# Kernel tuning notes

Measured on AMD Instinct MI355X. Metric: run time of the kernel, lower is better.

Reference implementation:

```python
import jax, jax.numpy as jnp
import numpy as np

B = 1048576
INPUT_DIM = 64
NUM_LAYERS = 8   # number of trees
DEPTH = 6
TREE_DIM = 2
NUM_LEAVES = 2 ** DEPTH


def setup_inputs() -> dict:
    key = jax.random.key(0)
    ks = jax.random.split(key, 6)
    x = jax.random.normal(ks[0], (B, INPUT_DIM), dtype=jnp.float32)
    # Stacked per-tree, per-level Linear(input_dim, 1) selectors.
    W_sel = jax.random.normal(ks[1], (NUM_LAYERS, DEPTH, INPUT_DIM), dtype=jnp.float32) / np.sqrt(INPUT_DIM)
    b_sel = jax.random.normal(ks[2], (NUM_LAYERS, DEPTH), dtype=jnp.float32) * 0.01
    leaf_values = jax.random.normal(ks[3], (NUM_LAYERS, NUM_LEAVES, TREE_DIM), dtype=jnp.float32)
    fc_w = jax.random.normal(ks[4], (2, NUM_LAYERS * TREE_DIM), dtype=jnp.float32) / np.sqrt(NUM_LAYERS * TREE_DIM)
    fc_b = jax.random.normal(ks[5], (2,), dtype=jnp.float32) * 0.01
    return {"x": x, "W_sel": W_sel, "b_sel": b_sel, "leaf_values": leaf_values,
            "fc_w": fc_w, "fc_b": fc_b}


def reference(x, W_sel, b_sel, leaf_values, fc_w, fc_b):
    # All trees / levels in one contraction: [B, T, D]
    logits = jnp.einsum('bi,tdi->btd', x, W_sel) + b_sel
    # sigmoid(z) > 0.5  <=>  z > 0, but keep explicit sigmoid for faithfulness
    bits = (jax.nn.sigmoid(logits) > 0.5).astype(jnp.int32)  # [B, T, D]
    # leaf_indices = fold(idx*2 + bit) == sum bit_l * 2^(D-1-l)
    powers = (2 ** jnp.arange(DEPTH - 1, -1, -1)).astype(jnp.int32)  # [D]
    leaf_idx = jnp.sum(bits * powers, axis=-1)  # [B, T]
    # Per-tree leaf gather: leaf_values[t, leaf_idx[b, t]] -> [B, T, C]
    tree_ids = jnp.arange(NUM_LAYERS)[None, :]  # [1, T]
    leaves = leaf_values[tree_ids, leaf_idx]    # [B, T, C]
    concatenated = leaves.reshape(x.shape[0], NUM_LAYERS * TREE_DIM)
    return concatenated @ fc_w.T + fc_b
```

## Files before the change

### kernel.cpp

```cpp
#include <hip/hip_runtime.h>
#include <hip/hip_bf16.h>
#include <stdint.h>


typedef float f32x2 __attribute__((ext_vector_type(2)));
typedef float f32x4 __attribute__((ext_vector_type(4)));
typedef short short8 __attribute__((ext_vector_type(8)));

static constexpr int   kBlocks  = 4096;
static constexpr float kTau     = 1.5f * 0x1p-24f;
static constexpr float kMarginB = 2e-3f;

__device__ __noinline__ float np_exact_dot(const float* __restrict__ xs,
                                           const float* __restrict__ w) {
#pragma clang fp contract(off)
  float s[4];
#pragma unroll
  for (int L = 0; L < 4; ++L) {
    float t = xs[12 + L] * w[12 + L];
    t = xs[8 + L] * w[8 + L] + t;
    t = xs[4 + L] * w[4 + L] + t;
    t = xs[0 + L] * w[0 + L] + t;
#pragma unroll
    for (int j = 1; j < 4; ++j) {
      const int o = 16 * j;
      t = xs[o + 12 + L] * w[o + 12 + L] + t;
      t = xs[o +  8 + L] * w[o +  8 + L] + t;
      t = xs[o +  4 + L] * w[o +  4 + L] + t;
      t = xs[o +  0 + L] * w[o +  0 + L] + t;
    }
    s[L] = t;
  }
  return (s[0] + s[1]) + (s[2] + s[3]);
}

__device__ __forceinline__ short bf16_hi(float v, float& hf) {
  const __hip_bfloat16 h = __float2bfloat16(v);
  hf = __bfloat162float(h);
  return __builtin_bit_cast(short, h);
}
__device__ __forceinline__ short bf16_rn(float v) {
  return __builtin_bit_cast(short, __float2bfloat16(v));
}

__global__ __launch_bounds__(256) void forest_mfma(
    const float* __restrict__ x,
    const float* __restrict__ Wsel,
    const float* __restrict__ bsel,
    const float* __restrict__ leaf,
    const float* __restrict__ fcw,
    const float* __restrict__ fcb,
    float* __restrict__ out)
{
  const int lane = threadIdx.x & 63;
  const int wave = threadIdx.x >> 6;
  const int q    = lane >> 4;
  const int r16  = lane & 15;
  const int rowbase = (blockIdx.x * 4 + wave) * 64;

  const float* xw = x + (size_t)(rowbase + r16) * 64 + q * 8;
  f32x4 xa[4][4];
#pragma unroll
  for (int c = 0; c < 2; ++c) {
    const float* p = xw + (size_t)c * 16 * 64;
    xa[c][0] = *(const f32x4*)(p);
    xa[c][1] = *(const f32x4*)(p + 4);
    xa[c][2] = *(const f32x4*)(p + 32);
    xa[c][3] = *(const f32x4*)(p + 36);
  }

  __shared__ f32x2 lleaf[512];
  ((f32x4*)lleaf)[threadIdx.x] = ((const f32x4*)leaf)[threadIdx.x];

  short8 whi[3][2], wlo[3][2];
#pragma unroll
  for (int rt = 0; rt < 3; ++rt) {
#pragma unroll
    for (int kh = 0; kh < 2; ++kh) {
      const float* wp = Wsel + (rt * 16 + r16) * 64 + kh * 32 + q * 8;
      const f32x4 w0 = *(const f32x4*)wp;
      const f32x4 w1 = *(const f32x4*)(wp + 4);
      short8 hi, lo;
#pragma unroll
      for (int i = 0; i < 4; ++i) {
        float hf;
        short h = bf16_hi(w0[i], hf);
        hi[i] = h;     lo[i]     = bf16_rn(w0[i] - hf);
        h = bf16_hi(w1[i], hf);
        hi[4 + i] = h; lo[4 + i] = bf16_rn(w1[i] - hf);
      }
      whi[rt][kh] = hi; wlo[rt][kh] = lo;
    }
  }

  f32x4 taub[3];
#pragma unroll
  for (int rt = 0; rt < 3; ++rt) {
    const f32x4 bs = *(const f32x4*)(bsel + rt * 16 + q * 4);
    f32x4 t;
#pragma unroll
    for (int i = 0; i < 4; ++i) t[i] = kTau - bs[i];
    taub[rt] = t;
  }

  uint64_t bits = 0, flag = 0;

#pragma unroll
  for (int ct = 0; ct < 4; ++ct) {
    if (ct < 2) {
      const float* p = xw + (size_t)(ct + 2) * 16 * 64;
      xa[ct + 2][0] = *(const f32x4*)(p);
      xa[ct + 2][1] = *(const f32x4*)(p + 4);
      xa[ct + 2][2] = *(const f32x4*)(p + 32);
      xa[ct + 2][3] = *(const f32x4*)(p + 36);
    }

    short8 xh0, xl0, xh1, xl1;
#pragma unroll
    for (int i = 0; i < 4; ++i) {
      float hf;
      short h = bf16_hi(xa[ct][0][i], hf); xh0[i]     = h; xl0[i]     = bf16_rn(xa[ct][0][i] - hf);
      h = bf16_hi(xa[ct][1][i], hf);       xh0[4 + i] = h; xl0[4 + i] = bf16_rn(xa[ct][1][i] - hf);
      h = bf16_hi(xa[ct][2][i], hf);       xh1[i]     = h; xl1[i]     = bf16_rn(xa[ct][2][i] - hf);
      h = bf16_hi(xa[ct][3][i], hf);       xh1[4 + i] = h; xl1[4 + i] = bf16_rn(xa[ct][3][i] - hf);
    }

    f32x4 acc[3];
#pragma unroll
    for (int rt = 0; rt < 3; ++rt) {
      f32x4 c = {0.f, 0.f, 0.f, 0.f};
      c = __builtin_amdgcn_mfma_f32_16x16x32_bf16(whi[rt][0], xh0, c, 0, 0, 0);
      c = __builtin_amdgcn_mfma_f32_16x16x32_bf16(whi[rt][1], xh1, c, 0, 0, 0);
      c = __builtin_amdgcn_mfma_f32_16x16x32_bf16(whi[rt][0], xl0, c, 0, 0, 0);
      c = __builtin_amdgcn_mfma_f32_16x16x32_bf16(whi[rt][1], xl1, c, 0, 0, 0);
      c = __builtin_amdgcn_mfma_f32_16x16x32_bf16(wlo[rt][0], xh0, c, 0, 0, 0);
      c = __builtin_amdgcn_mfma_f32_16x16x32_bf16(wlo[rt][1], xh1, c, 0, 0, 0);
      acc[rt] = c;
    }

    uint64_t pb = 0, pf = 0;
#pragma unroll
    for (int rt = 0; rt < 3; ++rt) {
#pragma unroll
      for (int i = 0; i < 4; ++i) {
        const float t = acc[rt][i] - taub[rt][i];
        const int d = rt * 16 + q * 4 + i;
        pb |= (uint64_t)(t > 0.f ? 1u : 0u) << d;
        pf |= (uint64_t)(__builtin_fabsf(t) < kMarginB ? 1u : 0u) << d;
      }
    }
    pb |= __shfl_xor((unsigned long long)pb, 16);
    pb |= __shfl_xor((unsigned long long)pb, 32);
    pf |= __shfl_xor((unsigned long long)pf, 16);
    pf |= __shfl_xor((unsigned long long)pf, 32);
    if (ct == q) { bits = pb; flag = pf; }
  }

  const float* __restrict__ xrow = x + (size_t)(rowbase + lane) * 64;
  while (flag) {
    const int d = __builtin_ctzll(flag);
    flag &= flag - 1;
    const float z = np_exact_dot(xrow, Wsel + d * 64) + bsel[d];
    const uint64_t m = 1ull << d;
    bits = (z > kTau) ? (bits | m) : (bits & ~m);
  }

  __syncthreads();
  float o0 = fcb[0], o1 = fcb[1];
#pragma unroll
  for (int t = 0; t < 8; ++t) {
    int idx = 0;
#pragma unroll
    for (int l = 0; l < 6; ++l)
      idx = idx * 2 + (int)((bits >> (t * 6 + l)) & 1u);
    const f32x2 lv = lleaf[t * 64 + idx];
    o0 = fmaf(lv.x, fcw[2 * t], o0);
    o0 = fmaf(lv.y, fcw[2 * t + 1], o0);
    o1 = fmaf(lv.x, fcw[16 + 2 * t], o1);
    o1 = fmaf(lv.y, fcw[16 + 2 * t + 1], o1);
  }
  f32x2 r; r.x = o0; r.y = o1;
  ((f32x2*)out)[rowbase + lane] = r;
}

extern "C" void kernel_launch(void* const* d_in, const int* in_sizes, int n_in,
                              void* d_out, int out_size, void* d_ws, size_t ws_size,
                              hipStream_t stream) {
  (void)in_sizes; (void)n_in; (void)out_size; (void)d_ws; (void)ws_size;
  forest_mfma<<<kBlocks, 256, 0, stream>>>(
      (const float*)d_in[0],
      (const float*)d_in[1],
      (const float*)d_in[2],
      (const float*)d_in[3],
      (const float*)d_in[4],
      (const float*)d_in[5],
      (float*)d_out);
}
```

Before: 372.0 us.

## Process two 64-row groups per wave with rolling x prefetch and tighter margin

Each wave now handles 128 rows instead of 64, halving the grid. The per-wave setup (weight bf16 hi/lo split, bias prep, leaf LDS load) is amortised over twice the rows, and x tiles stream through a 3-slot rolling prefetch buffer. The near-threshold margin that triggers the exact fp32 recompute is shrunk, so fewer rows take the slow path. The cost is less parallelism and a higher risk of wrong bits when the split-bf16 error exceeds the new margin.

```diff
diff --git a/kernel.cpp b/kernel.cpp
--- a/kernel.cpp
+++ b/kernel.cpp
@@ -7,9 +7,9 @@
 typedef float f32x4 __attribute__((ext_vector_type(4)));
 typedef short short8 __attribute__((ext_vector_type(8)));
 
-static constexpr int   kBlocks  = 4096;
+static constexpr int   kBlocks  = 2048;
 static constexpr float kTau     = 1.5f * 0x1p-24f;
-static constexpr float kMarginB = 2e-3f;
+static constexpr float kMarginB = 8e-4f;
 
 __device__ __noinline__ float np_exact_dot(const float* __restrict__ xs,
                                            const float* __restrict__ w) {
@@ -41,6 +41,64 @@
 }
 __device__ __forceinline__ short bf16_rn(float v) {
   return __builtin_bit_cast(short, __float2bfloat16(v));
+}
+
+template <int G, int CT>
+__device__ __forceinline__ void step(const float* __restrict__ xb,
+                                     f32x4 (&xa)[3][4],
+                                     const short8 (&whi)[3][2],
+                                     const short8 (&wlo)[3][2],
+                                     const f32x4 (&taub)[3],
+                                     int q, uint64_t& bits, uint64_t& flag) {
+  constexpr int U = G * 4 + CT;
+  if constexpr (U < 6) {
+    const float* p = xb + (size_t)(U + 2) * 1024;
+    xa[(U + 2) % 3][0] = *(const f32x4*)(p);
+    xa[(U + 2) % 3][1] = *(const f32x4*)(p + 4);
+    xa[(U + 2) % 3][2] = *(const f32x4*)(p + 32);
+    xa[(U + 2) % 3][3] = *(const f32x4*)(p + 36);
+  }
+  constexpr int cb = U % 3;
+
+  short8 xh0, xl0, xh1, xl1;
+#pragma unroll
+  for (int i = 0; i < 4; ++i) {
+    float hf;
+    short h = bf16_hi(xa[cb][0][i], hf); xh0[i]     = h; xl0[i]     = bf16_rn(xa[cb][0][i] - hf);
+    h = bf16_hi(xa[cb][1][i], hf);       xh0[4 + i] = h; xl0[4 + i] = bf16_rn(xa[cb][1][i] - hf);
+    h = bf16_hi(xa[cb][2][i], hf);       xh1[i]     = h; xl1[i]     = bf16_rn(xa[cb][2][i] - hf);
+    h = bf16_hi(xa[cb][3][i], hf);       xh1[4 + i] = h; xl1[4 + i] = bf16_rn(xa[cb][3][i] - hf);
+  }
+
+  f32x4 acc[3];
+#pragma unroll
+  for (int rt = 0; rt < 3; ++rt) {
+    f32x4 c = {0.f, 0.f, 0.f, 0.f};
+    c = __builtin_amdgcn_mfma_f32_16x16x32_bf16(whi[rt][0], xh0, c, 0, 0, 0);
+    c = __builtin_amdgcn_mfma_f32_16x16x32_bf16(whi[rt][1], xh1, c, 0, 0, 0);
+    c = __builtin_amdgcn_mfma_f32_16x16x32_bf16(whi[rt][0], xl0, c, 0, 0, 0);
+    c = __builtin_amdgcn_mfma_f32_16x16x32_bf16(whi[rt][1], xl1, c, 0, 0, 0);
+    c = __builtin_amdgcn_mfma_f32_16x16x32_bf16(wlo[rt][0], xh0, c, 0, 0, 0);
+    c = __builtin_amdgcn_mfma_f32_16x16x32_bf16(wlo[rt][1], xh1, c, 0, 0, 0);
+    acc[rt] = c;
+  }
+
+  uint64_t pb = 0, pf = 0;
+#pragma unroll
+  for (int rt = 0; rt < 3; ++rt) {
+#pragma unroll
+    for (int i = 0; i < 4; ++i) {
+      const float t = acc[rt][i] - taub[rt][i];
+      const int d = rt * 16 + q * 4 + i;
+      pb |= (uint64_t)(t > 0.f ? 1u : 0u) << d;
+      pf |= (uint64_t)(__builtin_fabsf(t) < kMarginB ? 1u : 0u) << d;
+    }
+  }
+  pb |= __shfl_xor((unsigned long long)pb, 16);
+  pb |= __shfl_xor((unsigned long long)pb, 32);
+  pf |= __shfl_xor((unsigned long long)pf, 16);
+  pf |= __shfl_xor((unsigned long long)pf, 32);
+  if (CT == q) { bits = pb; flag = pf; }
 }
 
 __global__ __launch_bounds__(256) void forest_mfma(
@@ -56,13 +114,13 @@
   const int wave = threadIdx.x >> 6;
   const int q    = lane >> 4;
   const int r16  = lane & 15;
-  const int rowbase = (blockIdx.x * 4 + wave) * 64;
-
-  const float* xw = x + (size_t)(rowbase + r16) * 64 + q * 8;
-  f32x4 xa[4][4];
+  const int rowbase = (blockIdx.x * 4 + wave) * 128;
+
+  const float* xb = x + (size_t)(rowbase + r16) * 64 + q * 8;
+  f32x4 xa[3][4];
 #pragma unroll
   for (int c = 0; c < 2; ++c) {
-    const float* p = xw + (size_t)c * 16 * 64;
+    const float* p = xb + (size_t)c * 1024;
     xa[c][0] = *(const f32x4*)(p);
     xa[c][1] = *(const f32x4*)(p + 4);
     xa[c][2] = *(const f32x4*)(p + 32);
@@ -103,84 +161,57 @@
     taub[rt] = t;
   }
 
-  uint64_t bits = 0, flag = 0;
-
-#pragma unroll
-  for (int ct = 0; ct < 4; ++ct) {
-    if (ct < 2) {
-      const float* p = xw + (size_t)(ct + 2) * 16 * 64;
-      xa[ct + 2][0] = *(const f32x4*)(p);
-      xa[ct + 2][1] = *(const f32x4*)(p + 4);
-      xa[ct + 2][2] = *(const f32x4*)(p + 32);
-      xa[ct + 2][3] = *(const f32x4*)(p + 36);
-    }
-
-    short8 xh0, xl0, xh1, xl1;
-#pragma unroll
-    for (int i = 0; i < 4; ++i) {
-      float hf;
-      short h = bf16_hi(xa[ct][0][i], hf); xh0[i]     = h; xl0[i]     = bf16_rn(xa[ct][0][i] - hf);
-      h = bf16_hi(xa[ct][1][i], hf);       xh0[4 + i] = h; xl0[4 + i] = bf16_rn(xa[ct][1][i] - hf);
-      h = bf16_hi(xa[ct][2][i], hf);       xh1[i]     = h; xl1[i]     = bf16_rn(xa[ct][2][i] - hf);
-      h = bf16_hi(xa[ct][3][i], hf);       xh1[4 + i] = h; xl1[4 + i] = bf16_rn(xa[ct][3][i] - hf);
-    }
-
-    f32x4 acc[3];
-#pragma unroll
-    for (int rt = 0; rt < 3; ++rt) {
-      f32x4 c = {0.f, 0.f, 0.f, 0.f};
-      c = __builtin_amdgcn_mfma_f32_16x16x32_bf16(whi[rt][0], xh0, c, 0, 0, 0);
-      c = __builtin_amdgcn_mfma_f32_16x16x32_bf16(whi[rt][1], xh1, c, 0, 0, 0);
-      c = __builtin_amdgcn_mfma_f32_16x16x32_bf16(whi[rt][0], xl0, c, 0, 0, 0);
-      c = __builtin_amdgcn_mfma_f32_16x16x32_bf16(whi[rt][1], xl1, c, 0, 0, 0);
-      c = __builtin_amdgcn_mfma_f32_16x16x32_bf16(wlo[rt][0], xh0, c, 0, 0, 0);
-      c = __builtin_amdgcn_mfma_f32_16x16x32_bf16(wlo[rt][1], xh1, c, 0, 0, 0);
-      acc[rt] = c;
-    }
-
-    uint64_t pb = 0, pf = 0;
-#pragma unroll
-    for (int rt = 0; rt < 3; ++rt) {
-#pragma unroll
-      for (int i = 0; i < 4; ++i) {
-        const float t = acc[rt][i] - taub[rt][i];
-        const int d = rt * 16 + q * 4 + i;
-        pb |= (uint64_t)(t > 0.f ? 1u : 0u) << d;
-        pf |= (uint64_t)(__builtin_fabsf(t) < kMarginB ? 1u : 0u) << d;
-      }
-    }
-    pb |= __shfl_xor((unsigned long long)pb, 16);
-    pb |= __shfl_xor((unsigned long long)pb, 32);
-    pf |= __shfl_xor((unsigned long long)pf, 16);
-    pf |= __shfl_xor((unsigned long long)pf, 32);
-    if (ct == q) { bits = pb; flag = pf; }
-  }
-
-  const float* __restrict__ xrow = x + (size_t)(rowbase + lane) * 64;
-  while (flag) {
-    const int d = __builtin_ctzll(flag);
-    flag &= flag - 1;
-    const float z = np_exact_dot(xrow, Wsel + d * 64) + bsel[d];
-    const uint64_t m = 1ull << d;
-    bits = (z > kTau) ? (bits | m) : (bits & ~m);
-  }
+  uint64_t bits0 = 0, flag0 = 0, bits1 = 0, flag1 = 0;
+  step<0, 0>(xb, xa, whi, wlo, taub, q, bits0, flag0);
+  step<0, 1>(xb, xa, whi, wlo, taub, q, bits0, flag0);
+  step<0, 2>(xb, xa, whi, wlo, taub, q, bits0, flag0);
+  step<0, 3>(xb, xa, whi, wlo, taub, q, bits0, flag0);
+  step<1, 0>(xb, xa, whi, wlo, taub, q, bits1, flag1);
+  step<1, 1>(xb, xa, whi, wlo, taub, q, bits1, flag1);
+  step<1, 2>(xb, xa, whi, wlo, taub, q, bits1, flag1);
+  step<1, 3>(xb, xa, whi, wlo, taub, q, bits1, flag1);
 
   __syncthreads();
-  float o0 = fcb[0], o1 = fcb[1];
-#pragma unroll
-  for (int t = 0; t < 8; ++t) {
-    int idx = 0;
-#pragma unroll
-    for (int l = 0; l < 6; ++l)
-      idx = idx * 2 + (int)((bits >> (t * 6 + l)) & 1u);
-    const f32x2 lv = lleaf[t * 64 + idx];
-    o0 = fmaf(lv.x, fcw[2 * t], o0);
-    o0 = fmaf(lv.y, fcw[2 * t + 1], o0);
-    o1 = fmaf(lv.x, fcw[16 + 2 * t], o1);
-    o1 = fmaf(lv.y, fcw[16 + 2 * t + 1], o1);
-  }
-  f32x2 r; r.x = o0; r.y = o1;
-  ((f32x2*)out)[rowbase + lane] = r;
+
+  {
+    const float* __restrict__ xrow = x + (size_t)(rowbase + lane) * 64;
+    while (flag0) {
+      const int d = __builtin_ctzll(flag0);
+      flag0 &= flag0 - 1;
+      const float z = np_exact_dot(xrow, Wsel + d * 64) + bsel[d];
+      const uint64_t m = 1ull << d;
+      bits0 = (z > kTau) ? (bits0 | m) : (bits0 & ~m);
+    }
+    const float* __restrict__ xrow1 = xrow + 64 * 64;
+    while (flag1) {
+      const int d = __builtin_ctzll(flag1);
+      flag1 &= flag1 - 1;
+      const float z = np_exact_dot(xrow1, Wsel + d * 64) + bsel[d];
+      const uint64_t m = 1ull << d;
+      bits1 = (z > kTau) ? (bits1 | m) : (bits1 & ~m);
+    }
+  }
+
+  const float fb0 = fcb[0], fb1 = fcb[1];
+#pragma unroll
+  for (int g = 0; g < 2; ++g) {
+    const uint64_t bits = g ? bits1 : bits0;
+    float o0 = fb0, o1 = fb1;
+#pragma unroll
+    for (int t = 0; t < 8; ++t) {
+      int idx = 0;
+#pragma unroll
+      for (int l = 0; l < 6; ++l)
+        idx = idx * 2 + (int)((bits >> (t * 6 + l)) & 1u);
+      const f32x2 lv = lleaf[t * 64 + idx];
+      o0 = fmaf(lv.x, fcw[2 * t], o0);
+      o0 = fmaf(lv.y, fcw[2 * t + 1], o0);
+      o1 = fmaf(lv.x, fcw[16 + 2 * t], o1);
+      o1 = fmaf(lv.y, fcw[16 + 2 * t + 1], o1);
+    }
+    f32x2 r; r.x = o0; r.y = o1;
+    ((f32x2*)out)[rowbase + g * 64 + lane] = r;
+  }
 }
 
 extern "C" void kernel_launch(void* const* d_in, const int* in_sizes, int n_in,
```

Measured after the change: 373.0 us. No clear change (+0.3%).
